# Kernel optimization log

Hardware: AMD Instinct MI355X
Metric: run time of the kernel (lower is better)

The kernel has to match this reference:

```python
import jax, jax.numpy as jnp
import numpy as np

N = 50000      # nodes
E = 800000     # edges
H = 64         # num_hidden
NUM_LAYERS = 4 # -> NUM_LAYERS-1 shared-weight processor steps
EPS = 1e-12


def _mlp3(x, w1, b1, w2, b2, w3, b3):
    h = jax.nn.relu(x @ w1 + b1)
    h = jax.nn.relu(h @ w2 + b2)
    return h @ w3 + b3


def setup_inputs() -> dict:
    key = jax.random.key(0)
    ks = jax.random.split(key, 32)

    def gl(k, shape):
        fan_in = shape[0]
        return (jax.random.normal(k, shape, jnp.float32) / np.sqrt(fan_in)).astype(jnp.float32)

    inp = {
        "X_curr": jax.random.normal(ks[0], (N, 6), jnp.float32),
        "y_prev": jax.random.normal(ks[1], (N,), jnp.float32),
        "edge": jax.random.randint(ks[2], (2, E), 0, N, dtype=jnp.int64),
        # edge net: Linear(9,H) ReLU Linear(H,H) ReLU Linear(H,3)
        "ew1": gl(ks[3], (9, H)), "eb1": jnp.zeros((H,), jnp.float32),
        "ew2": gl(ks[4], (H, H)), "eb2": jnp.zeros((H,), jnp.float32),
        "ew3": gl(ks[5], (H, 3)), "eb3": jnp.zeros((3,), jnp.float32),
        # node net: Linear(5,H) ReLU Linear(H,H) ReLU Linear(H,1)
        "nw1": gl(ks[6], (5, H)), "nb1": jnp.zeros((H,), jnp.float32),
        "nw2": gl(ks[7], (H, H)), "nb2": jnp.zeros((H,), jnp.float32),
        "nw3": gl(ks[8], (H, 1)), "nb3": jnp.zeros((1,), jnp.float32),
        # decoder: Linear(5,H) ReLU Linear(H,H) ReLU Linear(H,H) ReLU Linear(H,1)
        "dw1": gl(ks[9], (5, H)),  "db1": jnp.zeros((H,), jnp.float32),
        "dw2": gl(ks[10], (H, H)), "db2": jnp.zeros((H,), jnp.float32),
        "dw3": gl(ks[11], (H, H)), "db3": jnp.zeros((H,), jnp.float32),
        "dw4": gl(ks[12], (H, 1)), "db4": jnp.zeros((1,), jnp.float32),
        "mode": 0,
    }
    return inp


def reference(X_curr, y_prev, edge,
              ew1, eb1, ew2, eb2, ew3, eb3,
              nw1, nb1, nw2, nb2, nw3, nb3,
              dw1, db1, dw2, db2, dw3, db3, dw4, db4,
              mode):
    src, dst = edge[0], edge[1]
    n = X_curr.shape[0]

    # x_in: [N,5] = (pos x,y,z, feature col 4, y_prev)
    x_in = jnp.concatenate([X_curr[:, jnp.array([0, 1, 2, 4])], y_prev[:, None]], axis=-1)

    # initial edge_attr = (f_dest - f_src) * disp  -> [E,3]
    disp0 = x_in[dst, :3] - x_in[src, :3]
    f_r = x_in[dst, 4] - x_in[src, 4]
    edge_attr = f_r[:, None] * disp0

    cnt = jax.ops.segment_sum(jnp.ones((edge.shape[1], 1), x_in.dtype), dst, num_segments=n)
    denom = jnp.maximum(cnt, 1.0)

    for _ in range(NUM_LAYERS - 1):  # shared weights across processors
        xs = x_in[src]
        xd = x_in[dst]
        disp = xd[:, :3] - xs[:, :3]
        norm = jnp.sqrt(jnp.sum(disp * disp, axis=-1, keepdims=True) + EPS)
        net_in = jnp.concatenate([disp, norm, edge_attr, xs[:, 4:5], xd[:, 4:5]], axis=-1)  # [E,9]
        edge_attr = edge_attr + _mlp3(net_in, ew1, eb1, ew2, eb2, ew3, eb3)

        # scatter-mean of edge_attr at destination nodes
        aggr = jax.ops.segment_sum(edge_attr, dst, num_segments=n) / denom  # [N,3]
        node_in = jnp.concatenate([x_in[:, 3:5], aggr], axis=-1)            # [N,5]
        delta = _mlp3(node_in, nw1, nb1, nw2, nb2, nw3, nb3)[:, 0]
        x_in = jnp.concatenate([x_in[:, :4], (x_in[:, 4] + delta)[:, None]], axis=-1)

    # decoder
    h = jax.nn.relu(x_in @ dw1 + db1)
    h = jax.nn.relu(h @ dw2 + db2)
    h = jax.nn.relu(h @ dw3 + db3)
    x_out = h @ dw4 + db4  # [N,1]
    return y_prev + x_out[:, 0]
```

## Files before the change

### kernel.cpp

```cpp
#include <hip/hip_runtime.h>
#include <math.h>

#define N_NODES 50000
#define N_EDGES 800000
#define EPS 1e-12f
#define SCAN_NB 196
#define MAXB 6144

typedef __attribute__((ext_vector_type(8))) short bf16x8;
typedef __attribute__((ext_vector_type(4))) float f32x4;

__device__ inline unsigned pk_bf16(float a, float b) {
    unsigned ua = __float_as_uint(a), ub = __float_as_uint(b);
    ua = (ua + 0x7FFFu + ((ua >> 16) & 1u)) >> 16;
    ub = (ub + 0x7FFFu + ((ub >> 16) & 1u)) >> 16;
    return ua | (ub << 16);
}

#define W1OFF 0
#define W2OFF 4096
#define W3OFF 13312
#define RS 144
#define EB1 15616
#define EB2 15872
#define EB3 16128
#define EIMG_B 16192
#define DW1OFF 0
#define DW2OFF 4096
#define DW3OFF 13312
#define DW4OFF 22528
#define DB1 24832
#define DB2 25088
#define DB3 25344
#define DB4 25600
#define DIMG_B 25664

__global__ void k_node_init(const float* __restrict__ X, const float* __restrict__ yp,
                            float4* __restrict__ px4, float* __restrict__ f) {
    int n = blockIdx.x * blockDim.x + threadIdx.x;
    if (n < N_NODES) {
        px4[n] = make_float4(X[n * 6 + 0], X[n * 6 + 1], X[n * 6 + 2], X[n * 6 + 4]);
        f[n] = yp[n];
    }
}

__global__ __launch_bounds__(256) void k_prep(
    const float* __restrict__ ew1, const float* __restrict__ ew2,
    const float* __restrict__ ew3, const float* __restrict__ eb1,
    const float* __restrict__ eb2, const float* __restrict__ eb3,
    const float* __restrict__ nw1, const float* __restrict__ nw2,
    const float* __restrict__ nw3, const float* __restrict__ nb1,
    const float* __restrict__ nb2, const float* __restrict__ nb3,
    const float* __restrict__ dw1, const float* __restrict__ dw2,
    const float* __restrict__ dw3, const float* __restrict__ dw4,
    const float* __restrict__ db1, const float* __restrict__ db2,
    const float* __restrict__ db3, const float* __restrict__ db4,
    char* __restrict__ eimg, char* __restrict__ nimg, char* __restrict__ dimg) {
    const int t = threadIdx.x;
    const int n = t & 63, kg = t >> 6;
    const int n3 = t & 15, kg3 = t >> 4;
    if (blockIdx.x == 0) {
        unsigned pk[4];
#pragma unroll
        for (int i = 0; i < 4; i++) {
            int k0 = kg * 8 + i * 2;
            float v0 = (k0 < 9) ? ew1[k0 * 64 + n] : 0.f;
            float v1 = (k0 + 1 < 9) ? ew1[(k0 + 1) * 64 + n] : 0.f;
            pk[i] = pk_bf16(v0, v1);
        }
        *(uint4*)(eimg + W1OFF + n * 64 + kg * 16) = make_uint4(pk[0], pk[1], pk[2], pk[3]);
        unsigned pk2[8];
#pragma unroll
        for (int i = 0; i < 8; i++) {
            int k0 = kg * 16 + i * 2;
            pk2[i] = pk_bf16(ew2[k0 * 64 + n], ew2[(k0 + 1) * 64 + n]);
        }
        *(uint4*)(eimg + W2OFF + n * RS + kg * 32) = make_uint4(pk2[0], pk2[1], pk2[2], pk2[3]);
        *(uint4*)(eimg + W2OFF + n * RS + kg * 32 + 16) = make_uint4(pk2[4], pk2[5], pk2[6], pk2[7]);
        unsigned pk3[2];
#pragma unroll
        for (int i = 0; i < 2; i++) {
            int k0 = kg3 * 4 + i * 2;
            float v0 = (n3 < 3) ? ew3[k0 * 3 + n3] : 0.f;
            float v1 = (n3 < 3) ? ew3[(k0 + 1) * 3 + n3] : 0.f;
            pk3[i] = pk_bf16(v0, v1);
        }
        *(uint2*)(eimg + W3OFF + n3 * RS + kg3 * 8) = make_uint2(pk3[0], pk3[1]);
        if (t < 64) {
            ((float*)(eimg + EB1))[t] = eb1[t];
            ((float*)(eimg + EB2))[t] = eb2[t];
        }
        if (t < 16) ((float*)(eimg + EB3))[t] = (t < 3) ? eb3[t] : 0.f;
    } else if (blockIdx.x == 1) {
        unsigned pk[4];
#pragma unroll
        for (int i = 0; i < 4; i++) {
            int k0 = kg * 8 + i * 2;
            float v0 = (k0 < 5) ? nw1[k0 * 64 + n] : 0.f;
            float v1 = (k0 + 1 < 5) ? nw1[(k0 + 1) * 64 + n] : 0.f;
            pk[i] = pk_bf16(v0, v1);
        }
        *(uint4*)(nimg + W1OFF + n * 64 + kg * 16) = make_uint4(pk[0], pk[1], pk[2], pk[3]);
        unsigned pk2[8];
#pragma unroll
        for (int i = 0; i < 8; i++) {
            int k0 = kg * 16 + i * 2;
            pk2[i] = pk_bf16(nw2[k0 * 64 + n], nw2[(k0 + 1) * 64 + n]);
        }
        *(uint4*)(nimg + W2OFF + n * RS + kg * 32) = make_uint4(pk2[0], pk2[1], pk2[2], pk2[3]);
        *(uint4*)(nimg + W2OFF + n * RS + kg * 32 + 16) = make_uint4(pk2[4], pk2[5], pk2[6], pk2[7]);
        unsigned pk3[2];
#pragma unroll
        for (int i = 0; i < 2; i++) {
            int k0 = kg3 * 4 + i * 2;
            float v0 = (n3 == 0) ? nw3[k0] : 0.f;
            float v1 = (n3 == 0) ? nw3[k0 + 1] : 0.f;
            pk3[i] = pk_bf16(v0, v1);
        }
        *(uint2*)(nimg + W3OFF + n3 * RS + kg3 * 8) = make_uint2(pk3[0], pk3[1]);
        if (t < 64) {
            ((float*)(nimg + EB1))[t] = nb1[t];
            ((float*)(nimg + EB2))[t] = nb2[t];
        }
        if (t < 16) ((float*)(nimg + EB3))[t] = (t == 0) ? nb3[0] : 0.f;
    } else {
        unsigned pk[4];
#pragma unroll
        for (int i = 0; i < 4; i++) {
            int k0 = kg * 8 + i * 2;
            float v0 = (k0 < 5) ? dw1[k0 * 64 + n] : 0.f;
            float v1 = (k0 + 1 < 5) ? dw1[(k0 + 1) * 64 + n] : 0.f;
            pk[i] = pk_bf16(v0, v1);
        }
        *(uint4*)(dimg + DW1OFF + n * 64 + kg * 16) = make_uint4(pk[0], pk[1], pk[2], pk[3]);
        unsigned pk2[8], pk3b[8];
#pragma unroll
        for (int i = 0; i < 8; i++) {
            int k0 = kg * 16 + i * 2;
            pk2[i] = pk_bf16(dw2[k0 * 64 + n], dw2[(k0 + 1) * 64 + n]);
            pk3b[i] = pk_bf16(dw3[k0 * 64 + n], dw3[(k0 + 1) * 64 + n]);
        }
        *(uint4*)(dimg + DW2OFF + n * RS + kg * 32) = make_uint4(pk2[0], pk2[1], pk2[2], pk2[3]);
        *(uint4*)(dimg + DW2OFF + n * RS + kg * 32 + 16) = make_uint4(pk2[4], pk2[5], pk2[6], pk2[7]);
        *(uint4*)(dimg + DW3OFF + n * RS + kg * 32) = make_uint4(pk3b[0], pk3b[1], pk3b[2], pk3b[3]);
        *(uint4*)(dimg + DW3OFF + n * RS + kg * 32 + 16) = make_uint4(pk3b[4], pk3b[5], pk3b[6], pk3b[7]);
        unsigned pk4[2];
#pragma unroll
        for (int i = 0; i < 2; i++) {
            int k0 = kg3 * 4 + i * 2;
            float v0 = (n3 == 0) ? dw4[k0] : 0.f;
            float v1 = (n3 == 0) ? dw4[k0 + 1] : 0.f;
            pk4[i] = pk_bf16(v0, v1);
        }
        *(uint2*)(dimg + DW4OFF + n3 * RS + kg3 * 8) = make_uint2(pk4[0], pk4[1]);
        if (t < 64) {
            ((float*)(dimg + DB1))[t] = db1[t];
            ((float*)(dimg + DB2))[t] = db2[t];
            ((float*)(dimg + DB3))[t] = db3[t];
        }
        if (t < 16) ((float*)(dimg + DB4))[t] = (t == 0) ? db4[0] : 0.f;
    }
}

__global__ __launch_bounds__(256) void k_bucket(const int* __restrict__ edge,
                                                int* __restrict__ btail,
                                                int2* __restrict__ staging) {
    __shared__ int hist[256], loff[256], gbase[256], fill[256];
    __shared__ int2 ebL[2048];
    __shared__ unsigned short bktL[2048];
    const int t = threadIdx.x;
    const int base = blockIdx.x * 2048;
    const int cnt = min(2048, N_EDGES - base);
    hist[t] = 0; fill[t] = 0;
    __syncthreads();

    int2 my[8]; int mb[8];
#pragma unroll
    for (int j = 0; j < 8; j++) {
        int i = base + t + j * 256;
        if (i < N_EDGES) {
            int s = edge[i], d = edge[N_EDGES + i];
            my[j] = make_int2(s, d);
            mb[j] = d >> 8;
            atomicAdd(&hist[mb[j]], 1);
        } else mb[j] = -1;
    }
    __syncthreads();
    int v = hist[t];
    loff[t] = v;
    __syncthreads();
    for (int off = 1; off < 256; off <<= 1) {
        int x = (t >= off) ? loff[t - off] : 0;
        __syncthreads();
        loff[t] += x;
        __syncthreads();
    }
    int ex = loff[t] - v;
    __syncthreads();
    loff[t] = ex;
    if (v > 0) gbase[t] = atomicAdd(&btail[t], v);
    __syncthreads();
#pragma unroll
    for (int j = 0; j < 8; j++) {
        if (mb[j] >= 0) {
            int lp = loff[mb[j]] + atomicAdd(&fill[mb[j]], 1);
            ebL[lp] = my[j];
            bktL[lp] = (unsigned short)mb[j];
        }
    }
    __syncthreads();
    for (int i = t; i < cnt; i += 256) {
        int b = bktL[i];
        int gp = gbase[b] + (i - loff[b]);
        if (gp < MAXB) staging[b * MAXB + gp] = ebL[i];
    }
}

__global__ void k_bscan(const int* __restrict__ btail, int* __restrict__ bbase) {
    __shared__ int s[256];
    int t = threadIdx.x;
    int v = (t < SCAN_NB) ? btail[t] : 0;
    s[t] = v;
    __syncthreads();
    for (int off = 1; off < 256; off <<= 1) {
        int x = (t >= off) ? s[t - off] : 0;
        __syncthreads();
        s[t] += x;
        __syncthreads();
    }
    if (t < SCAN_NB) bbase[t] = s[t] - v;
}

__global__ __launch_bounds__(256) void k_bsort(const int2* __restrict__ staging,
                                               const int* __restrict__ btail,
                                               const int* __restrict__ bbase,
                                               int2* __restrict__ sd,
                                               int* __restrict__ rowptr) {
    __shared__ int hist[256], excl[256], fill[256], sbuf[256];
    __shared__ int2 ebL[MAXB];
    const int b = blockIdx.x, t = threadIdx.x;
    const int size = min(btail[b], MAXB);
    const int gb = bbase[b];
    for (int i = t; i < size; i += 256) ebL[i] = staging[b * MAXB + i];
    hist[t] = 0; fill[t] = 0;
    __syncthreads();
    for (int i = t; i < size; i += 256) atomicAdd(&hist[ebL[i].y & 255], 1);
    __syncthreads();
    int v = hist[t];
    sbuf[t] = v;
    __syncthreads();
    for (int off = 1; off < 256; off <<= 1) {
        int x = (t >= off) ? sbuf[t - off] : 0;
        __syncthreads();
        sbuf[t] += x;
        __syncthreads();
    }
    int ex = sbuf[t] - v;
    excl[t] = ex;
    int n = (b << 8) + t;
    if (n < N_NODES) rowptr[n] = gb + ex;
    if (b == SCAN_NB - 1 && t == 0) rowptr[N_NODES] = N_EDGES;
    __syncthreads();
    for (int i = t; i < size; i += 256) {
        int2 v2 = ebL[i];
        int ld = v2.y & 255;
        int pos = excl[ld] + atomicAdd(&fill[ld], 1);
        sd[gb + pos] = v2;
    }
}

__global__ void k_edge_init(const int2* __restrict__ sd,
                            const float4* __restrict__ px4,
                            const float* __restrict__ yp,
                            float4* __restrict__ dnrm, float4* __restrict__ ea) {
    int e = blockIdx.x * blockDim.x + threadIdx.x;
    if (e < N_EDGES) {
        int2 SD = sd[e];
        float4 ps = px4[SD.x], pd = px4[SD.y];
        float dx = pd.x - ps.x, dy = pd.y - ps.y, dz = pd.z - ps.z;
        float nrm = sqrtf(dx * dx + dy * dy + dz * dz + EPS);
        dnrm[e] = make_float4(dx, dy, dz, nrm);
        float fr = yp[SD.y] - yp[SD.x];
        ea[e] = make_float4(fr * dx, fr * dy, fr * dz, 0.f);
    }
}

__global__ __launch_bounds__(256, 2) void k_edge_mlp(
    const int2* __restrict__ sd, const float4* __restrict__ dnrm,
    float4* __restrict__ ea, const float* __restrict__ f,
    const char* __restrict__ eimg) {
    __shared__ __align__(16) char smem[EIMG_B + 4 * 64 * RS];
    const int t = threadIdx.x;
    const int lane = t & 63, wave = t >> 6;
    const int c = lane & 15, q = lane >> 4;

    for (int i = t; i < EIMG_B / 16; i += 256)
        ((uint4*)smem)[i] = ((const uint4*)eimg)[i];

    char* mybuf = smem + EIMG_B + wave * (64 * RS);
    const int e = blockIdx.x * 256 + t;
    int2 SD = sd[e];
    float4 DN = dnrm[e];
    float4 EA = ea[e];
    float fs = f[SD.x], fd = f[SD.y];
    {
        char* row = mybuf + lane * RS;
        *(uint4*)(row) = make_uint4(pk_bf16(DN.x, DN.y), pk_bf16(DN.z, DN.w),
                                    pk_bf16(EA.x, EA.y), pk_bf16(EA.z, fs));
        *(uint4*)(row + 16) = make_uint4(pk_bf16(fd, 0.f), 0u, 0u, 0u);
        *(uint4*)(row + 32) = make_uint4(0u, 0u, 0u, 0u);
        *(uint4*)(row + 48) = make_uint4(0u, 0u, 0u, 0u);
    }
    __syncthreads();

    bf16x8 Wa1[4], Wa2[8], Wa3[2];
#pragma unroll
    for (int mt = 0; mt < 4; mt++)
        Wa1[mt] = *(bf16x8*)(smem + W1OFF + (mt * 16 + c) * 64 + q * 16);
#pragma unroll
    for (int mt = 0; mt < 4; mt++)
#pragma unroll
        for (int ks = 0; ks < 2; ks++)
            Wa2[mt * 2 + ks] =
                *(bf16x8*)(smem + W2OFF + (mt * 16 + c) * RS + ks * 64 + q * 16);
#pragma unroll
    for (int ks = 0; ks < 2; ks++)
        Wa3[ks] = *(bf16x8*)(smem + W3OFF + c * RS + ks * 64 + q * 16);
    float4 b1v[4], b2v[4], b3v;
#pragma unroll
    for (int mt = 0; mt < 4; mt++) {
        b1v[mt] = *(const float4*)(smem + EB1 + (mt * 16 + q * 4) * 4);
        b2v[mt] = *(const float4*)(smem + EB2 + (mt * 16 + q * 4) * 4);
    }
    b3v = *(const float4*)(smem + EB3 + q * 16);

#pragma unroll
    for (int nt = 0; nt < 4; nt++) {
        char* rowb = mybuf + (nt * 16 + c) * RS;
        bf16x8 Eb = *(bf16x8*)(rowb + q * 16);
        f32x4 a1[4];
#pragma unroll
        for (int mt = 0; mt < 4; mt++) {
            a1[mt] = (f32x4){b1v[mt].x, b1v[mt].y, b1v[mt].z, b1v[mt].w};
            a1[mt] = __builtin_amdgcn_mfma_f32_16x16x32_bf16(Wa1[mt], Eb, a1[mt], 0, 0, 0);
        }
#pragma unroll
        for (int mt = 0; mt < 4; mt++)
            *(uint2*)(rowb + mt * 32 + q * 8) = make_uint2(
                pk_bf16(fmaxf(a1[mt][0], 0.f), fmaxf(a1[mt][1], 0.f)),
                pk_bf16(fmaxf(a1[mt][2], 0.f), fmaxf(a1[mt][3], 0.f)));
        bf16x8 H0 = *(bf16x8*)(rowb + q * 16);
        bf16x8 H1 = *(bf16x8*)(rowb + 64 + q * 16);
        f32x4 a2[4];
#pragma unroll
        for (int mt = 0; mt < 4; mt++) {
            a2[mt] = (f32x4){b2v[mt].x, b2v[mt].y, b2v[mt].z, b2v[mt].w};
            a2[mt] = __builtin_amdgcn_mfma_f32_16x16x32_bf16(Wa2[mt * 2 + 0], H0, a2[mt], 0, 0, 0);
            a2[mt] = __builtin_amdgcn_mfma_f32_16x16x32_bf16(Wa2[mt * 2 + 1], H1, a2[mt], 0, 0, 0);
        }
#pragma unroll
        for (int mt = 0; mt < 4; mt++)
            *(uint2*)(rowb + mt * 32 + q * 8) = make_uint2(
                pk_bf16(fmaxf(a2[mt][0], 0.f), fmaxf(a2[mt][1], 0.f)),
                pk_bf16(fmaxf(a2[mt][2], 0.f), fmaxf(a2[mt][3], 0.f)));
        bf16x8 G0 = *(bf16x8*)(rowb + q * 16);
        bf16x8 G1 = *(bf16x8*)(rowb + 64 + q * 16);
        f32x4 a3 = (f32x4){b3v.x, b3v.y, b3v.z, b3v.w};
        a3 = __builtin_amdgcn_mfma_f32_16x16x32_bf16(Wa3[0], G0, a3, 0, 0, 0);
        a3 = __builtin_amdgcn_mfma_f32_16x16x32_bf16(Wa3[1], G1, a3, 0, 0, 0);
        if (q == 0)
            *(float4*)(rowb + 128) = make_float4(a3[0], a3[1], a3[2], a3[3]);
    }

    float4 o = *(float4*)(mybuf + lane * RS + 128);
    ea[e] = make_float4(EA.x + o.x, EA.y + o.y, EA.z + o.z, 0.f);
}

__global__ __launch_bounds__(256, 2) void k_node_mlp(
    const float4* __restrict__ px4, float* __restrict__ f,
    const float4* __restrict__ ea, const int* __restrict__ rowptr,
    const char* __restrict__ nimg) {
    __shared__ __align__(16) char smem[EIMG_B + 4 * 64 * RS];
    const int t = threadIdx.x;
    const int lane = t & 63, wave = t >> 6;
    const int c = lane & 15, q = lane >> 4;

    for (int i = t; i < EIMG_B / 16; i += 256)
        ((uint4*)smem)[i] = ((const uint4*)nimg)[i];

    char* mybuf = smem + EIMG_B + wave * (64 * RS);
    const int idx = blockIdx.x * 256 + t;
    const int n = (idx < N_NODES) ? idx : (N_NODES - 1);

    int b0 = rowptr[n], b1 = rowptr[n + 1];
    float a0 = 0.f, a1s = 0.f, a2s = 0.f;
    for (int p = b0; p < b1; p++) {
        float4 v = ea[p];
        a0 += v.x; a1s += v.y; a2s += v.z;
    }
    float inv = 1.0f / fmaxf((float)(b1 - b0), 1.0f);
    float4 P = px4[n];
    float fn = f[n];
    {
        char* row = mybuf + lane * RS;
        *(uint4*)(row) = make_uint4(pk_bf16(P.w, fn), pk_bf16(a0 * inv, a1s * inv),
                                    pk_bf16(a2s * inv, 0.f), 0u);
        *(uint4*)(row + 16) = make_uint4(0u, 0u, 0u, 0u);
        *(uint4*)(row + 32) = make_uint4(0u, 0u, 0u, 0u);
        *(uint4*)(row + 48) = make_uint4(0u, 0u, 0u, 0u);
    }
    __syncthreads();

    bf16x8 Wa1[4], Wa2[8], Wa3[2];
#pragma unroll
    for (int mt = 0; mt < 4; mt++)
        Wa1[mt] = *(bf16x8*)(smem + W1OFF + (mt * 16 + c) * 64 + q * 16);
#pragma unroll
    for (int mt = 0; mt < 4; mt++)
#pragma unroll
        for (int ks = 0; ks < 2; ks++)
            Wa2[mt * 2 + ks] =
                *(bf16x8*)(smem + W2OFF + (mt * 16 + c) * RS + ks * 64 + q * 16);
#pragma unroll
    for (int ks = 0; ks < 2; ks++)
        Wa3[ks] = *(bf16x8*)(smem + W3OFF + c * RS + ks * 64 + q * 16);
    float4 b1v[4], b2v[4], b3v;
#pragma unroll
    for (int mt = 0; mt < 4; mt++) {
        b1v[mt] = *(const float4*)(smem + EB1 + (mt * 16 + q * 4) * 4);
        b2v[mt] = *(const float4*)(smem + EB2 + (mt * 16 + q * 4) * 4);
    }
    b3v = *(const float4*)(smem + EB3 + q * 16);

#pragma unroll
    for (int nt = 0; nt < 4; nt++) {
        char* rowb = mybuf + (nt * 16 + c) * RS;
        bf16x8 Eb = *(bf16x8*)(rowb + q * 16);
        f32x4 a1v[4];
#pragma unroll
        for (int mt = 0; mt < 4; mt++) {
            a1v[mt] = (f32x4){b1v[mt].x, b1v[mt].y, b1v[mt].z, b1v[mt].w};
            a1v[mt] = __builtin_amdgcn_mfma_f32_16x16x32_bf16(Wa1[mt], Eb, a1v[mt], 0, 0, 0);
        }
#pragma unroll
        for (int mt = 0; mt < 4; mt++)
            *(uint2*)(rowb + mt * 32 + q * 8) = make_uint2(
                pk_bf16(fmaxf(a1v[mt][0], 0.f), fmaxf(a1v[mt][1], 0.f)),
                pk_bf16(fmaxf(a1v[mt][2], 0.f), fmaxf(a1v[mt][3], 0.f)));
        bf16x8 H0 = *(bf16x8*)(rowb + q * 16);
        bf16x8 H1 = *(bf16x8*)(rowb + 64 + q * 16);
        f32x4 a2v[4];
#pragma unroll
        for (int mt = 0; mt < 4; mt++) {
            a2v[mt] = (f32x4){b2v[mt].x, b2v[mt].y, b2v[mt].z, b2v[mt].w};
            a2v[mt] = __builtin_amdgcn_mfma_f32_16x16x32_bf16(Wa2[mt * 2 + 0], H0, a2v[mt], 0, 0, 0);
            a2v[mt] = __builtin_amdgcn_mfma_f32_16x16x32_bf16(Wa2[mt * 2 + 1], H1, a2v[mt], 0, 0, 0);
        }
#pragma unroll
        for (int mt = 0; mt < 4; mt++)
            *(uint2*)(rowb + mt * 32 + q * 8) = make_uint2(
                pk_bf16(fmaxf(a2v[mt][0], 0.f), fmaxf(a2v[mt][1], 0.f)),
                pk_bf16(fmaxf(a2v[mt][2], 0.f), fmaxf(a2v[mt][3], 0.f)));
        bf16x8 G0 = *(bf16x8*)(rowb + q * 16);
        bf16x8 G1 = *(bf16x8*)(rowb + 64 + q * 16);
        f32x4 a3 = (f32x4){b3v.x, b3v.y, b3v.z, b3v.w};
        a3 = __builtin_amdgcn_mfma_f32_16x16x32_bf16(Wa3[0], G0, a3, 0, 0, 0);
        a3 = __builtin_amdgcn_mfma_f32_16x16x32_bf16(Wa3[1], G1, a3, 0, 0, 0);
        if (q == 0) *(float*)(rowb + 128) = a3[0];
    }

    float o = *(float*)(mybuf + lane * RS + 128);
    if (idx < N_NODES) f[n] = fn + o;
}

__global__ __launch_bounds__(256, 2) void k_decoder(
    const float4* __restrict__ px4, const float* __restrict__ f,
    const float* __restrict__ yp, const char* __restrict__ dimg,
    float* __restrict__ out) {
    __shared__ __align__(16) char smem[DIMG_B + 4 * 64 * RS];
    const int t = threadIdx.x;
    const int lane = t & 63, wave = t >> 6;
    const int c = lane & 15, q = lane >> 4;

    for (int i = t; i < DIMG_B / 16; i += 256)
        ((uint4*)smem)[i] = ((const uint4*)dimg)[i];

    char* mybuf = smem + DIMG_B + wave * (64 * RS);
    const int idx = blockIdx.x * 256 + t;
    const int n = (idx < N_NODES) ? idx : (N_NODES - 1);
    float4 P = px4[n];
    float fn = f[n];
    {
        char* row = mybuf + lane * RS;
        *(uint4*)(row) = make_uint4(pk_bf16(P.x, P.y), pk_bf16(P.z, P.w),
                                    pk_bf16(fn, 0.f), 0u);
        *(uint4*)(row + 16) = make_uint4(0u, 0u, 0u, 0u);
        *(uint4*)(row + 32) = make_uint4(0u, 0u, 0u, 0u);
        *(uint4*)(row + 48) = make_uint4(0u, 0u, 0u, 0u);
    }
    __syncthreads();

    bf16x8 Wa1[4], Wa2[8], Wa3[8], Wa4[2];
#pragma unroll
    for (int mt = 0; mt < 4; mt++)
        Wa1[mt] = *(bf16x8*)(smem + DW1OFF + (mt * 16 + c) * 64 + q * 16);
#pragma unroll
    for (int mt = 0; mt < 4; mt++)
#pragma unroll
        for (int ks = 0; ks < 2; ks++) {
            Wa2[mt * 2 + ks] =
                *(bf16x8*)(smem + DW2OFF + (mt * 16 + c) * RS + ks * 64 + q * 16);
            Wa3[mt * 2 + ks] =
                *(bf16x8*)(smem + DW3OFF + (mt * 16 + c) * RS + ks * 64 + q * 16);
        }
#pragma unroll
    for (int ks = 0; ks < 2; ks++)
        Wa4[ks] = *(bf16x8*)(smem + DW4OFF + c * RS + ks * 64 + q * 16);
    float4 b1v[4], b2v[4], b3v[4], b4v;
#pragma unroll
    for (int mt = 0; mt < 4; mt++) {
        b1v[mt] = *(const float4*)(smem + DB1 + (mt * 16 + q * 4) * 4);
        b2v[mt] = *(const float4*)(smem + DB2 + (mt * 16 + q * 4) * 4);
        b3v[mt] = *(const float4*)(smem + DB3 + (mt * 16 + q * 4) * 4);
    }
    b4v = *(const float4*)(smem + DB4 + q * 16);

#pragma unroll
    for (int nt = 0; nt < 4; nt++) {
        char* rowb = mybuf + (nt * 16 + c) * RS;
        bf16x8 Eb = *(bf16x8*)(rowb + q * 16);
        f32x4 a1v[4];
#pragma unroll
        for (int mt = 0; mt < 4; mt++) {
            a1v[mt] = (f32x4){b1v[mt].x, b1v[mt].y, b1v[mt].z, b1v[mt].w};
            a1v[mt] = __builtin_amdgcn_mfma_f32_16x16x32_bf16(Wa1[mt], Eb, a1v[mt], 0, 0, 0);
        }
#pragma unroll
        for (int mt = 0; mt < 4; mt++)
            *(uint2*)(rowb + mt * 32 + q * 8) = make_uint2(
                pk_bf16(fmaxf(a1v[mt][0], 0.f), fmaxf(a1v[mt][1], 0.f)),
                pk_bf16(fmaxf(a1v[mt][2], 0.f), fmaxf(a1v[mt][3], 0.f)));
        bf16x8 H0 = *(bf16x8*)(rowb + q * 16);
        bf16x8 H1 = *(bf16x8*)(rowb + 64 + q * 16);
        f32x4 a2v[4];
#pragma unroll
        for (int mt = 0; mt < 4; mt++) {
            a2v[mt] = (f32x4){b2v[mt].x, b2v[mt].y, b2v[mt].z, b2v[mt].w};
            a2v[mt] = __builtin_amdgcn_mfma_f32_16x16x32_bf16(Wa2[mt * 2 + 0], H0, a2v[mt], 0, 0, 0);
            a2v[mt] = __builtin_amdgcn_mfma_f32_16x16x32_bf16(Wa2[mt * 2 + 1], H1, a2v[mt], 0, 0, 0);
        }
#pragma unroll
        for (int mt = 0; mt < 4; mt++)
            *(uint2*)(rowb + mt * 32 + q * 8) = make_uint2(
                pk_bf16(fmaxf(a2v[mt][0], 0.f), fmaxf(a2v[mt][1], 0.f)),
                pk_bf16(fmaxf(a2v[mt][2], 0.f), fmaxf(a2v[mt][3], 0.f)));
        bf16x8 G0 = *(bf16x8*)(rowb + q * 16);
        bf16x8 G1 = *(bf16x8*)(rowb + 64 + q * 16);
        f32x4 a3v[4];
#pragma unroll
        for (int mt = 0; mt < 4; mt++) {
            a3v[mt] = (f32x4){b3v[mt].x, b3v[mt].y, b3v[mt].z, b3v[mt].w};
            a3v[mt] = __builtin_amdgcn_mfma_f32_16x16x32_bf16(Wa3[mt * 2 + 0], G0, a3v[mt], 0, 0, 0);
            a3v[mt] = __builtin_amdgcn_mfma_f32_16x16x32_bf16(Wa3[mt * 2 + 1], G1, a3v[mt], 0, 0, 0);
        }
#pragma unroll
        for (int mt = 0; mt < 4; mt++)
            *(uint2*)(rowb + mt * 32 + q * 8) = make_uint2(
                pk_bf16(fmaxf(a3v[mt][0], 0.f), fmaxf(a3v[mt][1], 0.f)),
                pk_bf16(fmaxf(a3v[mt][2], 0.f), fmaxf(a3v[mt][3], 0.f)));
        bf16x8 F0 = *(bf16x8*)(rowb + q * 16);
        bf16x8 F1 = *(bf16x8*)(rowb + 64 + q * 16);
        f32x4 a4 = (f32x4){b4v.x, b4v.y, b4v.z, b4v.w};
        a4 = __builtin_amdgcn_mfma_f32_16x16x32_bf16(Wa4[0], F0, a4, 0, 0, 0);
        a4 = __builtin_amdgcn_mfma_f32_16x16x32_bf16(Wa4[1], F1, a4, 0, 0, 0);
        if (q == 0) *(float*)(rowb + 128) = a4[0];
    }

    float o = *(float*)(mybuf + lane * RS + 128);
    if (idx < N_NODES) out[n] = yp[n] + o;
}

extern "C" void kernel_launch(void* const* d_in, const int* in_sizes, int n_in,
                              void* d_out, int out_size, void* d_ws, size_t ws_size,
                              hipStream_t stream) {
    const float* X    = (const float*)d_in[0];
    const float* yp   = (const float*)d_in[1];
    const int*   edge = (const int*)d_in[2];
    const float *ew1 = (const float*)d_in[3],  *eb1 = (const float*)d_in[4];
    const float *ew2 = (const float*)d_in[5],  *eb2 = (const float*)d_in[6];
    const float *ew3 = (const float*)d_in[7],  *eb3 = (const float*)d_in[8];
    const float *nw1 = (const float*)d_in[9],  *nb1 = (const float*)d_in[10];
    const float *nw2 = (const float*)d_in[11], *nb2 = (const float*)d_in[12];
    const float *nw3 = (const float*)d_in[13], *nb3 = (const float*)d_in[14];
    const float *dw1 = (const float*)d_in[15], *db1 = (const float*)d_in[16];
    const float *dw2 = (const float*)d_in[17], *db2 = (const float*)d_in[18];
    const float *dw3 = (const float*)d_in[19], *db3 = (const float*)d_in[20];
    const float *dw4 = (const float*)d_in[21], *db4 = (const float*)d_in[22];
    float* out = (float*)d_out;

    char* p = (char*)d_ws;
    auto carve = [&](size_t bytes) {
        char* r = p;
        p += (bytes + 255) & ~(size_t)255;
        return r;
    };
    int2*   sd     = (int2*)  carve(sizeof(int2)   * N_EDGES);
    float4* dnrm   = (float4*)carve(sizeof(float4) * N_EDGES);
    float4* ea     = (float4*)carve(sizeof(float4) * N_EDGES);
    float4* px4    = (float4*)carve(sizeof(float4) * N_NODES);
    float*  f      = (float*) carve(sizeof(float)  * N_NODES);
    int*    rowptr = (int*)   carve(sizeof(int)    * (N_NODES + 1));
    int*    btail  = (int*)   carve(sizeof(int)    * 256);
    int*    bbase  = (int*)   carve(sizeof(int)    * 256);
    char*   eimg   = (char*)  carve(EIMG_B);
    char*   nimg   = (char*)  carve(EIMG_B);
    char*   dimg   = (char*)  carve(DIMG_B);
    int2*   staging = (int2*)dnrm;

    const int nb_n = SCAN_NB;
    const int nb_e = (N_EDGES + 255) / 256;
    const int nb_b = (N_EDGES + 2047) / 2048;

    hipMemsetAsync(btail, 0, sizeof(int) * 256, stream);
    k_node_init<<<nb_n, 256, 0, stream>>>(X, yp, px4, f);
    k_prep<<<3, 256, 0, stream>>>(ew1, ew2, ew3, eb1, eb2, eb3,
                                  nw1, nw2, nw3, nb1, nb2, nb3,
                                  dw1, dw2, dw3, dw4, db1, db2, db3, db4,
                                  eimg, nimg, dimg);
    k_bucket<<<nb_b, 256, 0, stream>>>(edge, btail, staging);
    k_bscan<<<1, 256, 0, stream>>>(btail, bbase);
    k_bsort<<<SCAN_NB, 256, 0, stream>>>(staging, btail, bbase, sd, rowptr);
    k_edge_init<<<nb_e, 256, 0, stream>>>(sd, px4, yp, dnrm, ea);

    for (int it = 0; it < 3; ++it) {
        k_edge_mlp<<<nb_e, 256, 0, stream>>>(sd, dnrm, ea, f, eimg);
        k_node_mlp<<<nb_n, 256, 0, stream>>>(px4, f, ea, rowptr, nimg);
    }
    k_decoder<<<nb_n, 256, 0, stream>>>(px4, f, yp, dimg, out);
}
```

Baseline: 280.6 us.

## Fuse setup kernels and read MLP weights from global instead of LDS

Merges node init with weight prep into one launch, folds the bucket scan into k_bsort, and computes the initial edge displacement/attr inside k_bsort, removing k_bscan and k_edge_init. Staging now gets its own buffer because dnrm is written during the sort. The MLP kernels no longer copy weight images into shared memory; weights and biases are read directly from global/L1/L2, shrinking LDS so edge_mlp can request 4 blocks per CU. The trade-off is redundant scans per block and more global/cache traffic for weights inside the MLP loops.

```diff
diff --git a/kernel.cpp b/kernel.cpp
--- a/kernel.cpp
+++ b/kernel.cpp
@@ -35,16 +35,9 @@
 #define DB4 25600
 #define DIMG_B 25664
 
-__global__ void k_node_init(const float* __restrict__ X, const float* __restrict__ yp,
-                            float4* __restrict__ px4, float* __restrict__ f) {
-    int n = blockIdx.x * blockDim.x + threadIdx.x;
-    if (n < N_NODES) {
-        px4[n] = make_float4(X[n * 6 + 0], X[n * 6 + 1], X[n * 6 + 2], X[n * 6 + 4]);
-        f[n] = yp[n];
-    }
-}
-
-__global__ __launch_bounds__(256) void k_prep(
+__global__ __launch_bounds__(256) void k_init(
+    const float* __restrict__ X, const float* __restrict__ yp,
+    float4* __restrict__ px4, float* __restrict__ f,
     const float* __restrict__ ew1, const float* __restrict__ ew2,
     const float* __restrict__ ew3, const float* __restrict__ eb1,
     const float* __restrict__ eb2, const float* __restrict__ eb3,
@@ -57,6 +50,14 @@
     const float* __restrict__ db3, const float* __restrict__ db4,
     char* __restrict__ eimg, char* __restrict__ nimg, char* __restrict__ dimg) {
     const int t = threadIdx.x;
+    if (blockIdx.x >= 3) {
+        int n = (blockIdx.x - 3) * 256 + t;
+        if (n < N_NODES) {
+            px4[n] = make_float4(X[n * 6 + 0], X[n * 6 + 1], X[n * 6 + 2], X[n * 6 + 4]);
+            f[n] = yp[n];
+        }
+        return;
+    }
     const int n = t & 63, kg = t >> 6;
     const int n3 = t & 15, kg3 = t >> 4;
     if (blockIdx.x == 0) {
@@ -216,38 +217,20 @@
     }
 }
 
-__global__ void k_bscan(const int* __restrict__ btail, int* __restrict__ bbase) {
-    __shared__ int s[256];
-    int t = threadIdx.x;
-    int v = (t < SCAN_NB) ? btail[t] : 0;
-    s[t] = v;
-    __syncthreads();
-    for (int off = 1; off < 256; off <<= 1) {
-        int x = (t >= off) ? s[t - off] : 0;
-        __syncthreads();
-        s[t] += x;
-        __syncthreads();
-    }
-    if (t < SCAN_NB) bbase[t] = s[t] - v;
-}
-
 __global__ __launch_bounds__(256) void k_bsort(const int2* __restrict__ staging,
                                                const int* __restrict__ btail,
-                                               const int* __restrict__ bbase,
+                                               const float4* __restrict__ px4,
+                                               const float* __restrict__ yp,
                                                int2* __restrict__ sd,
+                                               float4* __restrict__ dnrm,
+                                               float4* __restrict__ ea,
                                                int* __restrict__ rowptr) {
     __shared__ int hist[256], excl[256], fill[256], sbuf[256];
     __shared__ int2 ebL[MAXB];
     const int b = blockIdx.x, t = threadIdx.x;
-    const int size = min(btail[b], MAXB);
-    const int gb = bbase[b];
-    for (int i = t; i < size; i += 256) ebL[i] = staging[b * MAXB + i];
-    hist[t] = 0; fill[t] = 0;
-    __syncthreads();
-    for (int i = t; i < size; i += 256) atomicAdd(&hist[ebL[i].y & 255], 1);
-    __syncthreads();
-    int v = hist[t];
-    sbuf[t] = v;
+
+    int bv = (t < SCAN_NB) ? btail[t] : 0;
+    sbuf[t] = bv;
     __syncthreads();
     for (int off = 1; off < 256; off <<= 1) {
         int x = (t >= off) ? sbuf[t - off] : 0;
@@ -255,6 +238,23 @@
         sbuf[t] += x;
         __syncthreads();
     }
+    const int gb = (b == 0) ? 0 : sbuf[b - 1];
+    const int size = min(btail[b], MAXB);
+
+    for (int i = t; i < size; i += 256) ebL[i] = staging[b * MAXB + i];
+    hist[t] = 0; fill[t] = 0;
+    __syncthreads();
+    for (int i = t; i < size; i += 256) atomicAdd(&hist[ebL[i].y & 255], 1);
+    __syncthreads();
+    int v = hist[t];
+    sbuf[t] = v;
+    __syncthreads();
+    for (int off = 1; off < 256; off <<= 1) {
+        int x = (t >= off) ? sbuf[t - off] : 0;
+        __syncthreads();
+        sbuf[t] += x;
+        __syncthreads();
+    }
     int ex = sbuf[t] - v;
     excl[t] = ex;
     int n = (b << 8) + t;
@@ -265,39 +265,27 @@
         int2 v2 = ebL[i];
         int ld = v2.y & 255;
         int pos = excl[ld] + atomicAdd(&fill[ld], 1);
-        sd[gb + pos] = v2;
-    }
-}
-
-__global__ void k_edge_init(const int2* __restrict__ sd,
-                            const float4* __restrict__ px4,
-                            const float* __restrict__ yp,
-                            float4* __restrict__ dnrm, float4* __restrict__ ea) {
-    int e = blockIdx.x * blockDim.x + threadIdx.x;
-    if (e < N_EDGES) {
-        int2 SD = sd[e];
-        float4 ps = px4[SD.x], pd = px4[SD.y];
+        int gp = gb + pos;
+        sd[gp] = v2;
+        float4 ps = px4[v2.x], pd = px4[v2.y];
         float dx = pd.x - ps.x, dy = pd.y - ps.y, dz = pd.z - ps.z;
         float nrm = sqrtf(dx * dx + dy * dy + dz * dz + EPS);
-        dnrm[e] = make_float4(dx, dy, dz, nrm);
-        float fr = yp[SD.y] - yp[SD.x];
-        ea[e] = make_float4(fr * dx, fr * dy, fr * dz, 0.f);
-    }
-}
-
-__global__ __launch_bounds__(256, 2) void k_edge_mlp(
+        dnrm[gp] = make_float4(dx, dy, dz, nrm);
+        float fr = yp[v2.y] - yp[v2.x];
+        ea[gp] = make_float4(fr * dx, fr * dy, fr * dz, 0.f);
+    }
+}
+
+__global__ __launch_bounds__(256, 4) void k_edge_mlp(
     const int2* __restrict__ sd, const float4* __restrict__ dnrm,
     float4* __restrict__ ea, const float* __restrict__ f,
     const char* __restrict__ eimg) {
-    __shared__ __align__(16) char smem[EIMG_B + 4 * 64 * RS];
+    __shared__ __align__(16) char smem[4 * 64 * RS];
     const int t = threadIdx.x;
     const int lane = t & 63, wave = t >> 6;
     const int c = lane & 15, q = lane >> 4;
 
-    for (int i = t; i < EIMG_B / 16; i += 256)
-        ((uint4*)smem)[i] = ((const uint4*)eimg)[i];
-
-    char* mybuf = smem + EIMG_B + wave * (64 * RS);
+    char* mybuf = smem + wave * (64 * RS);
     const int e = blockIdx.x * 256 + t;
     int2 SD = sd[e];
     float4 DN = dnrm[e];
@@ -313,26 +301,16 @@
     }
     __syncthreads();
 
-    bf16x8 Wa1[4], Wa2[8], Wa3[2];
+    bf16x8 Wa1[4], Wa2[8];
 #pragma unroll
     for (int mt = 0; mt < 4; mt++)
-        Wa1[mt] = *(bf16x8*)(smem + W1OFF + (mt * 16 + c) * 64 + q * 16);
+        Wa1[mt] = *(const bf16x8*)(eimg + W1OFF + (mt * 16 + c) * 64 + q * 16);
 #pragma unroll
     for (int mt = 0; mt < 4; mt++)
 #pragma unroll
         for (int ks = 0; ks < 2; ks++)
             Wa2[mt * 2 + ks] =
-                *(bf16x8*)(smem + W2OFF + (mt * 16 + c) * RS + ks * 64 + q * 16);
-#pragma unroll
-    for (int ks = 0; ks < 2; ks++)
-        Wa3[ks] = *(bf16x8*)(smem + W3OFF + c * RS + ks * 64 + q * 16);
-    float4 b1v[4], b2v[4], b3v;
-#pragma unroll
-    for (int mt = 0; mt < 4; mt++) {
-        b1v[mt] = *(const float4*)(smem + EB1 + (mt * 16 + q * 4) * 4);
-        b2v[mt] = *(const float4*)(smem + EB2 + (mt * 16 + q * 4) * 4);
-    }
-    b3v = *(const float4*)(smem + EB3 + q * 16);
+                *(const bf16x8*)(eimg + W2OFF + (mt * 16 + c) * RS + ks * 64 + q * 16);
 
 #pragma unroll
     for (int nt = 0; nt < 4; nt++) {
@@ -341,7 +319,8 @@
         f32x4 a1[4];
 #pragma unroll
         for (int mt = 0; mt < 4; mt++) {
-            a1[mt] = (f32x4){b1v[mt].x, b1v[mt].y, b1v[mt].z, b1v[mt].w};
+            float4 bb = *(const float4*)(eimg + EB1 + (mt * 16 + q * 4) * 4);
+            a1[mt] = (f32x4){bb.x, bb.y, bb.z, bb.w};
             a1[mt] = __builtin_amdgcn_mfma_f32_16x16x32_bf16(Wa1[mt], Eb, a1[mt], 0, 0, 0);
         }
 #pragma unroll
@@ -354,7 +333,8 @@
         f32x4 a2[4];
 #pragma unroll
         for (int mt = 0; mt < 4; mt++) {
-            a2[mt] = (f32x4){b2v[mt].x, b2v[mt].y, b2v[mt].z, b2v[mt].w};
+            float4 bb = *(const float4*)(eimg + EB2 + (mt * 16 + q * 4) * 4);
+            a2[mt] = (f32x4){bb.x, bb.y, bb.z, bb.w};
             a2[mt] = __builtin_amdgcn_mfma_f32_16x16x32_bf16(Wa2[mt * 2 + 0], H0, a2[mt], 0, 0, 0);
             a2[mt] = __builtin_amdgcn_mfma_f32_16x16x32_bf16(Wa2[mt * 2 + 1], H1, a2[mt], 0, 0, 0);
         }
@@ -365,9 +345,12 @@
                 pk_bf16(fmaxf(a2[mt][2], 0.f), fmaxf(a2[mt][3], 0.f)));
         bf16x8 G0 = *(bf16x8*)(rowb + q * 16);
         bf16x8 G1 = *(bf16x8*)(rowb + 64 + q * 16);
-        f32x4 a3 = (f32x4){b3v.x, b3v.y, b3v.z, b3v.w};
-        a3 = __builtin_amdgcn_mfma_f32_16x16x32_bf16(Wa3[0], G0, a3, 0, 0, 0);
-        a3 = __builtin_amdgcn_mfma_f32_16x16x32_bf16(Wa3[1], G1, a3, 0, 0, 0);
+        bf16x8 W30 = *(const bf16x8*)(eimg + W3OFF + c * RS + q * 16);
+        bf16x8 W31 = *(const bf16x8*)(eimg + W3OFF + c * RS + 64 + q * 16);
+        float4 b3 = *(const float4*)(eimg + EB3 + q * 16);
+        f32x4 a3 = (f32x4){b3.x, b3.y, b3.z, b3.w};
+        a3 = __builtin_amdgcn_mfma_f32_16x16x32_bf16(W30, G0, a3, 0, 0, 0);
+        a3 = __builtin_amdgcn_mfma_f32_16x16x32_bf16(W31, G1, a3, 0, 0, 0);
         if (q == 0)
             *(float4*)(rowb + 128) = make_float4(a3[0], a3[1], a3[2], a3[3]);
     }
@@ -380,15 +363,12 @@
     const float4* __restrict__ px4, float* __restrict__ f,
     const float4* __restrict__ ea, const int* __restrict__ rowptr,
     const char* __restrict__ nimg) {
-    __shared__ __align__(16) char smem[EIMG_B + 4 * 64 * RS];
+    __shared__ __align__(16) char smem[4 * 64 * RS];
     const int t = threadIdx.x;
     const int lane = t & 63, wave = t >> 6;
     const int c = lane & 15, q = lane >> 4;
 
-    for (int i = t; i < EIMG_B / 16; i += 256)
-        ((uint4*)smem)[i] = ((const uint4*)nimg)[i];
-
-    char* mybuf = smem + EIMG_B + wave * (64 * RS);
+    char* mybuf = smem + wave * (64 * RS);
     const int idx = blockIdx.x * 256 + t;
     const int n = (idx < N_NODES) ? idx : (N_NODES - 1);
 
@@ -411,61 +391,56 @@
     }
     __syncthreads();
 
-    bf16x8 Wa1[4], Wa2[8], Wa3[2];
+    bf16x8 Wa1[4], Wa2[8];
 #pragma unroll
     for (int mt = 0; mt < 4; mt++)
-        Wa1[mt] = *(bf16x8*)(smem + W1OFF + (mt * 16 + c) * 64 + q * 16);
+        Wa1[mt] = *(const bf16x8*)(nimg + W1OFF + (mt * 16 + c) * 64 + q * 16);
 #pragma unroll
     for (int mt = 0; mt < 4; mt++)
 #pragma unroll
         for (int ks = 0; ks < 2; ks++)
             Wa2[mt * 2 + ks] =
-                *(bf16x8*)(smem + W2OFF + (mt * 16 + c) * RS + ks * 64 + q * 16);
-#pragma unroll
-    for (int ks = 0; ks < 2; ks++)
-        Wa3[ks] = *(bf16x8*)(smem + W3OFF + c * RS + ks * 64 + q * 16);
-    float4 b1v[4], b2v[4], b3v;
-#pragma unroll
-    for (int mt = 0; mt < 4; mt++) {
-        b1v[mt] = *(const float4*)(smem + EB1 + (mt * 16 + q * 4) * 4);
-        b2v[mt] = *(const float4*)(smem + EB2 + (mt * 16 + q * 4) * 4);
-    }
-    b3v = *(const float4*)(smem + EB3 + q * 16);
+                *(const bf16x8*)(nimg + W2OFF + (mt * 16 + c) * RS + ks * 64 + q * 16);
 
 #pragma unroll
     for (int nt = 0; nt < 4; nt++) {
         char* rowb = mybuf + (nt * 16 + c) * RS;
         bf16x8 Eb = *(bf16x8*)(rowb + q * 16);
-        f32x4 a1v[4];
+        f32x4 a1[4];
 #pragma unroll
         for (int mt = 0; mt < 4; mt++) {
-            a1v[mt] = (f32x4){b1v[mt].x, b1v[mt].y, b1v[mt].z, b1v[mt].w};
-            a1v[mt] = __builtin_amdgcn_mfma_f32_16x16x32_bf16(Wa1[mt], Eb, a1v[mt], 0, 0, 0);
+            float4 bb = *(const float4*)(nimg + EB1 + (mt * 16 + q * 4) * 4);
+            a1[mt] = (f32x4){bb.x, bb.y, bb.z, bb.w};
+            a1[mt] = __builtin_amdgcn_mfma_f32_16x16x32_bf16(Wa1[mt], Eb, a1[mt], 0, 0, 0);
         }
 #pragma unroll
         for (int mt = 0; mt < 4; mt++)
             *(uint2*)(rowb + mt * 32 + q * 8) = make_uint2(
-                pk_bf16(fmaxf(a1v[mt][0], 0.f), fmaxf(a1v[mt][1], 0.f)),
-                pk_bf16(fmaxf(a1v[mt][2], 0.f), fmaxf(a1v[mt][3], 0.f)));
+                pk_bf16(fmaxf(a1[mt][0], 0.f), fmaxf(a1[mt][1], 0.f)),
+                pk_bf16(fmaxf(a1[mt][2], 0.f), fmaxf(a1[mt][3], 0.f)));
         bf16x8 H0 = *(bf16x8*)(rowb + q * 16);
         bf16x8 H1 = *(bf16x8*)(rowb + 64 + q * 16);
-        f32x4 a2v[4];
+        f32x4 a2[4];
 #pragma unroll
         for (int mt = 0; mt < 4; mt++) {
-            a2v[mt] = (f32x4){b2v[mt].x, b2v[mt].y, b2v[mt].z, b2v[mt].w};
-            a2v[mt] = __builtin_amdgcn_mfma_f32_16x16x32_bf16(Wa2[mt * 2 + 0], H0, a2v[mt], 0, 0, 0);
-            a2v[mt] = __builtin_amdgcn_mfma_f32_16x16x32_bf16(Wa2[mt * 2 + 1], H1, a2v[mt], 0, 0, 0);
+            float4 bb = *(const float4*)(nimg + EB2 + (mt * 16 + q * 4) * 4);
+            a2[mt] = (f32x4){bb.x, bb.y, bb.z, bb.w};
+            a2[mt] = __builtin_amdgcn_mfma_f32_16x16x32_bf16(Wa2[mt * 2 + 0], H0, a2[mt], 0, 0, 0);
+            a2[mt] = __builtin_amdgcn_mfma_f32_16x16x32_bf16(Wa2[mt * 2 + 1], H1, a2[mt], 0, 0, 0);
         }
 #pragma unroll
         for (int mt = 0; mt < 4; mt++)
             *(uint2*)(rowb + mt * 32 + q * 8) = make_uint2(
-                pk_bf16(fmaxf(a2v[mt][0], 0.f), fmaxf(a2v[mt][1], 0.f)),
-                pk_bf16(fmaxf(a2v[mt][2], 0.f), fmaxf(a2v[mt][3], 0.f)));
+                pk_bf16(fmaxf(a2[mt][0], 0.f), fmaxf(a2[mt][1], 0.f)),
+                pk_bf16(fmaxf(a2[mt][2], 0.f), fmaxf(a2[mt][3], 0.f)));
         bf16x8 G0 = *(bf16x8*)(rowb + q * 16);
         bf16x8 G1 = *(bf16x8*)(rowb + 64 + q * 16);
-        f32x4 a3 = (f32x4){b3v.x, b3v.y, b3v.z, b3v.w};
-        a3 = __builtin_amdgcn_mfma_f32_16x16x32_bf16(Wa3[0], G0, a3, 0, 0, 0);
-        a3 = __builtin_amdgcn_mfma_f32_16x16x32_bf16(Wa3[1], G1, a3, 0, 0, 0);
+        bf16x8 W30 = *(const bf16x8*)(nimg + W3OFF + c * RS + q * 16);
+        bf16x8 W31 = *(const bf16x8*)(nimg + W3OFF + c * RS + 64 + q * 16);
+        float4 b3 = *(const float4*)(nimg + EB3 + q * 16);
+        f32x4 a3 = (f32x4){b3.x, b3.y, b3.z, b3.w};
+        a3 = __builtin_amdgcn_mfma_f32_16x16x32_bf16(W30, G0, a3, 0, 0, 0);
+        a3 = __builtin_amdgcn_mfma_f32_16x16x32_bf16(W31, G1, a3, 0, 0, 0);
         if (q == 0) *(float*)(rowb + 128) = a3[0];
     }
 
@@ -477,15 +452,12 @@
     const float4* __restrict__ px4, const float* __restrict__ f,
     const float* __restrict__ yp, const char* __restrict__ dimg,
     float* __restrict__ out) {
-    __shared__ __align__(16) char smem[DIMG_B + 4 * 64 * RS];
+    __shared__ __align__(16) char smem[4 * 64 * RS];
     const int t = threadIdx.x;
     const int lane = t & 63, wave = t >> 6;
     const int c = lane & 15, q = lane >> 4;
 
-    for (int i = t; i < DIMG_B / 16; i += 256)
-        ((uint4*)smem)[i] = ((const uint4*)dimg)[i];
-
-    char* mybuf = smem + DIMG_B + wave * (64 * RS);
+    char* mybuf = smem + wave * (64 * RS);
     const int idx = blockIdx.x * 256 + t;
     const int n = (idx < N_NODES) ? idx : (N_NODES - 1);
     float4 P = px4[n];
@@ -500,79 +472,74 @@
     }
     __syncthreads();
 
-    bf16x8 Wa1[4], Wa2[8], Wa3[8], Wa4[2];
+    bf16x8 Wa1[4], Wa2[8], Wa3[8];
 #pragma unroll
     for (int mt = 0; mt < 4; mt++)
-        Wa1[mt] = *(bf16x8*)(smem + DW1OFF + (mt * 16 + c) * 64 + q * 16);
+        Wa1[mt] = *(const bf16x8*)(dimg + DW1OFF + (mt * 16 + c) * 64 + q * 16);
 #pragma unroll
     for (int mt = 0; mt < 4; mt++)
 #pragma unroll
         for (int ks = 0; ks < 2; ks++) {
             Wa2[mt * 2 + ks] =
-                *(bf16x8*)(smem + DW2OFF + (mt * 16 + c) * RS + ks * 64 + q * 16);
+                *(const bf16x8*)(dimg + DW2OFF + (mt * 16 + c) * RS + ks * 64 + q * 16);
             Wa3[mt * 2 + ks] =
-                *(bf16x8*)(smem + DW3OFF + (mt * 16 + c) * RS + ks * 64 + q * 16);
-        }
-#pragma unroll
-    for (int ks = 0; ks < 2; ks++)
-        Wa4[ks] = *(bf16x8*)(smem + DW4OFF + c * RS + ks * 64 + q * 16);
-    float4 b1v[4], b2v[4], b3v[4], b4v;
-#pragma unroll
-    for (int mt = 0; mt < 4; mt++) {
-        b1v[mt] = *(const float4*)(smem + DB1 + (mt * 16 + q * 4) * 4);
-        b2v[mt] = *(const float4*)(smem + DB2 + (mt * 16 + q * 4) * 4);
-        b3v[mt] = *(const float4*)(smem + DB3 + (mt * 16 + q * 4) * 4);
-    }
-    b4v = *(const float4*)(smem + DB4 + q * 16);
+                *(const bf16x8*)(dimg + DW3OFF + (mt * 16 + c) * RS + ks * 64 + q * 16);
+        }
 
 #pragma unroll
     for (int nt = 0; nt < 4; nt++) {
         char* rowb = mybuf + (nt * 16 + c) * RS;
         bf16x8 Eb = *(bf16x8*)(rowb + q * 16);
-        f32x4 a1v[4];
+        f32x4 a1[4];
 #pragma unroll
         for (int mt = 0; mt < 4; mt++) {
-            a1v[mt] = (f32x4){b1v[mt].x, b1v[mt].y, b1v[mt].z, b1v[mt].w};
-            a1v[mt] = __builtin_amdgcn_mfma_f32_16x16x32_bf16(Wa1[mt], Eb, a1v[mt], 0, 0, 0);
+            float4 bb = *(const float4*)(dimg + DB1 + (mt * 16 + q * 4) * 4);
+            a1[mt] = (f32x4){bb.x, bb.y, bb.z, bb.w};
+            a1[mt] = __builtin_amdgcn_mfma_f32_16x16x32_bf16(Wa1[mt], Eb, a1[mt], 0, 0, 0);
         }
 #pragma unroll
         for (int mt = 0; mt < 4; mt++)
             *(uint2*)(rowb + mt * 32 + q * 8) = make_uint2(
-                pk_bf16(fmaxf(a1v[mt][0], 0.f), fmaxf(a1v[mt][1], 0.f)),
-                pk_bf16(fmaxf(a1v[mt][2], 0.f), fmaxf(a1v[mt][3], 0.f)));
+                pk_bf16(fmaxf(a1[mt][0], 0.f), fmaxf(a1[mt][1], 0.f)),
+                pk_bf16(fmaxf(a1[mt][2], 0.f), fmaxf(a1[mt][3], 0.f)));
         bf16x8 H0 = *(bf16x8*)(rowb + q * 16);
         bf16x8 H1 = *(bf16x8*)(rowb + 64 + q * 16);
-        f32x4 a2v[4];
+        f32x4 a2[4];
 #pragma unroll
         for (int mt = 0; mt < 4; mt++) {
-            a2v[mt] = (f32x4){b2v[mt].x, b2v[mt].y, b2v[mt].z, b2v[mt].w};
-            a2v[mt] = __builtin_amdgcn_mfma_f32_16x16x32_bf16(Wa2[mt * 2 + 0], H0, a2v[mt], 0, 0, 0);
-            a2v[mt] = __builtin_amdgcn_mfma_f32_16x16x32_bf16(Wa2[mt * 2 + 1], H1, a2v[mt], 0, 0, 0);
+            float4 bb = *(const float4*)(dimg + DB2 + (mt * 16 + q * 4) * 4);
+            a2[mt] = (f32x4){bb.x, bb.y, bb.z, bb.w};
+            a2[mt] = __builtin_amdgcn_mfma_f32_16x16x32_bf16(Wa2[mt * 2 + 0], H0, a2[mt], 0, 0, 0);
+            a2[mt] = __builtin_amdgcn_mfma_f32_16x16x32_bf16(Wa2[mt * 2 + 1], H1, a2[mt], 0, 0, 0);
         }
 #pragma unroll
         for (int mt = 0; mt < 4; mt++)
             *(uint2*)(rowb + mt * 32 + q * 8) = make_uint2(
-                pk_bf16(fmaxf(a2v[mt][0], 0.f), fmaxf(a2v[mt][1], 0.f)),
-                pk_bf16(fmaxf(a2v[mt][2], 0.f), fmaxf(a2v[mt][3], 0.f)));
+                pk_bf16(fmaxf(a2[mt][0], 0.f), fmaxf(a2[mt][1], 0.f)),
+                pk_bf16(fmaxf(a2[mt][2], 0.f), fmaxf(a2[mt][3], 0.f)));
         bf16x8 G0 = *(bf16x8*)(rowb + q * 16);
         bf16x8 G1 = *(bf16x8*)(rowb + 64 + q * 16);
-        f32x4 a3v[4];
+        f32x4 a3[4];
 #pragma unroll
         for (int mt = 0; mt < 4; mt++) {
-            a3v[mt] = (f32x4){b3v[mt].x, b3v[mt].y, b3v[mt].z, b3v[mt].w};
-            a3v[mt] = __builtin_amdgcn_mfma_f32_16x16x32_bf16(Wa3[mt * 2 + 0], G0, a3v[mt], 0, 0, 0);
-            a3v[mt] = __builtin_amdgcn_mfma_f32_16x16x32_bf16(Wa3[mt * 2 + 1], G1, a3v[mt], 0, 0, 0);
+            float4 bb = *(const float4*)(dimg + DB3 + (mt * 16 + q * 4) * 4);
+            a3[mt] = (f32x4){bb.x, bb.y, bb.z, bb.w};
+            a3[mt] = __builtin_amdgcn_mfma_f32_16x16x32_bf16(Wa3[mt * 2 + 0], G0, a3[mt], 0, 0, 0);
+            a3[mt] = __builtin_amdgcn_mfma_f32_16x16x32_bf16(Wa3[mt * 2 + 1], G1, a3[mt], 0, 0, 0);
         }
 #pragma unroll
         for (int mt = 0; mt < 4; mt++)
             *(uint2*)(rowb + mt * 32 + q * 8) = make_uint2(
-                pk_bf16(fmaxf(a3v[mt][0], 0.f), fmaxf(a3v[mt][1], 0.f)),
-                pk_bf16(fmaxf(a3v[mt][2], 0.f), fmaxf(a3v[mt][3], 0.f)));
+                pk_bf16(fmaxf(a3[mt][0], 0.f), fmaxf(a3[mt][1], 0.f)),
+                pk_bf16(fmaxf(a3[mt][2], 0.f), fmaxf(a3[mt][3], 0.f)));
         bf16x8 F0 = *(bf16x8*)(rowb + q * 16);
         bf16x8 F1 = *(bf16x8*)(rowb + 64 + q * 16);
-        f32x4 a4 = (f32x4){b4v.x, b4v.y, b4v.z, b4v.w};
-        a4 = __builtin_amdgcn_mfma_f32_16x16x32_bf16(Wa4[0], F0, a4, 0, 0, 0);
-        a4 = __builtin_amdgcn_mfma_f32_16x16x32_bf16(Wa4[1], F1, a4, 0, 0, 0);
+        bf16x8 W40 = *(const bf16x8*)(dimg + DW4OFF + c * RS + q * 16);
+        bf16x8 W41 = *(const bf16x8*)(dimg + DW4OFF + c * RS + 64 + q * 16);
+        float4 b4 = *(const float4*)(dimg + DB4 + q * 16);
+        f32x4 a4 = (f32x4){b4.x, b4.y, b4.z, b4.w};
+        a4 = __builtin_amdgcn_mfma_f32_16x16x32_bf16(W40, F0, a4, 0, 0, 0);
+        a4 = __builtin_amdgcn_mfma_f32_16x16x32_bf16(W41, F1, a4, 0, 0, 0);
         if (q == 0) *(float*)(rowb + 128) = a4[0];
     }
 
@@ -604,33 +571,31 @@
         p += (bytes + 255) & ~(size_t)255;
         return r;
     };
-    int2*   sd     = (int2*)  carve(sizeof(int2)   * N_EDGES);
-    float4* dnrm   = (float4*)carve(sizeof(float4) * N_EDGES);
-    float4* ea     = (float4*)carve(sizeof(float4) * N_EDGES);
-    float4* px4    = (float4*)carve(sizeof(float4) * N_NODES);
-    float*  f      = (float*) carve(sizeof(float)  * N_NODES);
-    int*    rowptr = (int*)   carve(sizeof(int)    * (N_NODES + 1));
-    int*    btail  = (int*)   carve(sizeof(int)    * 256);
-    int*    bbase  = (int*)   carve(sizeof(int)    * 256);
-    char*   eimg   = (char*)  carve(EIMG_B);
-    char*   nimg   = (char*)  carve(EIMG_B);
-    char*   dimg   = (char*)  carve(DIMG_B);
-    int2*   staging = (int2*)dnrm;
+    int2*   sd      = (int2*)  carve(sizeof(int2)   * N_EDGES);
+    float4* dnrm    = (float4*)carve(sizeof(float4) * N_EDGES);
+    float4* ea      = (float4*)carve(sizeof(float4) * N_EDGES);
+    int2*   staging = (int2*)  carve(sizeof(int2)   * SCAN_NB * MAXB);
+    float4* px4     = (float4*)carve(sizeof(float4) * N_NODES);
+    float*  f       = (float*) carve(sizeof(float)  * N_NODES);
+    int*    rowptr  = (int*)   carve(sizeof(int)    * (N_NODES + 1));
+    int*    btail   = (int*)   carve(sizeof(int)    * 256);
+    char*   eimg    = (char*)  carve(EIMG_B);
+    char*   nimg    = (char*)  carve(EIMG_B);
+    char*   dimg    = (char*)  carve(DIMG_B);
 
     const int nb_n = SCAN_NB;
     const int nb_e = (N_EDGES + 255) / 256;
     const int nb_b = (N_EDGES + 2047) / 2048;
 
     hipMemsetAsync(btail, 0, sizeof(int) * 256, stream);
-    k_node_init<<<nb_n, 256, 0, stream>>>(X, yp, px4, f);
-    k_prep<<<3, 256, 0, stream>>>(ew1, ew2, ew3, eb1, eb2, eb3,
-                                  nw1, nw2, nw3, nb1, nb2, nb3,
-                                  dw1, dw2, dw3, dw4, db1, db2, db3, db4,
-                                  eimg, nimg, dimg);
+    k_init<<<3 + nb_n, 256, 0, stream>>>(X, yp, px4, f,
+                                         ew1, ew2, ew3, eb1, eb2, eb3,
+                                         nw1, nw2, nw3, nb1, nb2, nb3,
+                                         dw1, dw2, dw3, dw4, db1, db2, db3, db4,
+                                         eimg, nimg, dimg);
     k_bucket<<<nb_b, 256, 0, stream>>>(edge, btail, staging);
-    k_bscan<<<1, 256, 0, stream>>>(btail, bbase);
-    k_bsort<<<SCAN_NB, 256, 0, stream>>>(staging, btail, bbase, sd, rowptr);
-    k_edge_init<<<nb_e, 256, 0, stream>>>(sd, px4, yp, dnrm, ea);
+    k_bsort<<<nb_n, 256, 0, stream>>>(staging, btail, px4, yp,
+                                      sd, dnrm, ea, rowptr);
 
     for (int it = 0; it < 3; ++it) {
         k_edge_mlp<<<nb_e, 256, 0, stream>>>(sd, dnrm, ea, f, eimg);
```

After: 295.4 us. 5.3% more time.
